# Kernel optimization log

Measured on AMD Instinct MI355X. Metric: run time of the kernel, lower is better.

## Reference

```python
import jax, jax.numpy as jnp
import numpy as np

KS = 7       # neighborhood kernel size (fixed in __init__)
HEADS = 8    # num_heads (fixed in __init__)
LN_EPS = 1e-5


def _nbr_idx(L, k):
    # NATTEN-style clamped window: window start shifts inward at borders (no padding)
    starts = jnp.clip(jnp.arange(L) - k // 2, 0, L - k)
    idx = starts[:, None] + jnp.arange(k)            # [L, k] absolute neighbor coords
    rel = idx - jnp.arange(L)[:, None] + (k - 1)     # [L, k] rel-pos-bias index in [0, 2k-2]
    return idx, rel


def _na2d(x, qkv_w, qkv_b, proj_w, proj_b, rpb):
    # x: [B, H, W, C]  -> neighborhood attention with clamped 7x7 windows
    B, H, W, C = x.shape
    hd = C // HEADS
    qkv = x @ qkv_w.T + qkv_b                        # [B,H,W,3C]
    q, k, v = jnp.split(qkv, 3, axis=-1)
    q = q.reshape(B, H, W, HEADS, hd) * (hd ** -0.5)
    k = k.reshape(B, H, W, HEADS, hd)
    v = v.reshape(B, H, W, HEADS, hd)
    ri, rri = _nbr_idx(H, KS)                        # [H,KS]
    ci, rci = _nbr_idx(W, KS)                        # [W,KS]
    # gather neighborhoods: [B,H,W,KS,KS,heads,hd]
    kn = k[:, ri[:, None, :, None], ci[None, :, None, :]]
    vn = v[:, ri[:, None, :, None], ci[None, :, None, :]]
    scores = jnp.einsum('bijhd,bijpqhd->bhijpq', q, kn)   # [B,heads,H,W,KS,KS]
    bias = rpb[:, rri[:, None, :, None], rci[None, :, None, :]]  # [heads,H,W,KS,KS]
    scores = scores + bias[None]
    attn = jax.nn.softmax(scores.reshape(B, HEADS, H, W, KS * KS), axis=-1)
    vn = vn.reshape(B, H, W, KS * KS, HEADS, hd)
    out = jnp.einsum('bhijp,bijphd->bijhd', attn, vn)      # [B,H,W,heads,hd]
    out = out.reshape(B, H, W, C)
    return out @ proj_w.T + proj_b


def _layernorm(x, g, b):
    mu = jnp.mean(x, axis=-1, keepdims=True)
    var = jnp.mean((x - mu) ** 2, axis=-1, keepdims=True)
    return (x - mu) * jax.lax.rsqrt(var + LN_EPS) * g + b


def setup_inputs() -> dict:
    key = jax.random.key(0)
    ks = jax.random.split(key, 4)
    B, T, H, W, C = 2, 8, 48, 48, 64
    return {
        'q': jax.random.normal(ks[0], (B, T, H, W, C), dtype=jnp.float32),
        'qkv_w': jax.random.normal(ks[1], (3 * C, C), dtype=jnp.float32) * 0.02,
        'qkv_b': jnp.zeros((3 * C,), jnp.float32),
        'proj_w': jax.random.normal(ks[2], (C, C), dtype=jnp.float32) * 0.02,
        'proj_b': jnp.zeros((C,), jnp.float32),
        'rpb': jax.random.normal(ks[3], (HEADS, 2 * KS - 1, 2 * KS - 1), dtype=jnp.float32) * 0.02,
        'ln_g': jnp.ones((C,), jnp.float32),
        'ln_b': jnp.zeros((C,), jnp.float32),
    }


def reference(q, qkv_w, qkv_b, proj_w, proj_b, rpb, ln_g, ln_b):
    B, T, H, W, C = q.shape
    x = q.reshape(B * T, H, W, C)                    # '(b t) h w c'
    x = _na2d(x, qkv_w, qkv_b, proj_w, proj_b, rpb)  # wPT path
    x = x.reshape(B, T, H, W, C)
    return _layernorm(x, ln_g, ln_b)                 # norm_q; wGC=False
```

## Files before the change

kernel.cpp:

```cpp
#include <hip/hip_runtime.h>
#include <hip/hip_bf16.h>

#define IH   48
#define IW   48
#define CH   64
#define KS   7
#define LN_EPS 1e-5f
#define QSCALE 0.35355339059327373f

#define TS   8
#define HS   14
#define HP   196
#define KVS  128
#define AOS  72

typedef __bf16 bf16_t;
typedef bf16_t bf16x8 __attribute__((ext_vector_type(8)));
typedef float  f32x4  __attribute__((ext_vector_type(4)));
typedef float  f32x2  __attribute__((ext_vector_type(2)));

__device__ __forceinline__ float bflo(unsigned u) { union { unsigned i; float f; } v; v.i = u << 16; return v.f; }
__device__ __forceinline__ float bfhi(unsigned u) { union { unsigned i; float f; } v; v.i = u & 0xffff0000u; return v.f; }
__device__ __forceinline__ f32x2 unp2(unsigned u) { f32x2 r; r.x = bflo(u); r.y = bfhi(u); return r; }

__device__ __forceinline__ float4 ldf4u(const float* p) {
    float4 r; __builtin_memcpy(&r, p, 16); return r;
}

__device__ __forceinline__ bf16x8 pack_bf16x8(float4 lo, float4 hi) {
    bf16x8 r;
    r[0] = (bf16_t)lo.x; r[1] = (bf16_t)lo.y; r[2] = (bf16_t)lo.z; r[3] = (bf16_t)lo.w;
    r[4] = (bf16_t)hi.x; r[5] = (bf16_t)hi.y; r[6] = (bf16_t)hi.z; r[7] = (bf16_t)hi.w;
    return r;
}

__global__ __launch_bounds__(256, 2) void fused_na_kernel(
        const float* __restrict__ x,
        const float* __restrict__ w,
        const float* __restrict__ b,
        const float* __restrict__ rpb,
        const float* __restrict__ pw,
        const float* __restrict__ pb,
        const float* __restrict__ g,
        const float* __restrict__ beta,
        float* __restrict__ out) {
    __shared__ __align__(16) __hip_bfloat16 kv[HP * KVS];
    __shared__ __align__(16) __hip_bfloat16 qao[64 * AOS];

    const int blk  = blockIdx.x;
    const int n    = blk & 15;
    const int tile = blk >> 4;
    const int i0   = (tile / 6) * TS;
    const int j0   = (tile % 6) * TS;
    int h0 = i0 - 3; h0 = h0 < 0 ? 0 : (h0 > IH - HS ? IH - HS : h0);
    int w0 = j0 - 3; w0 = w0 < 0 ? 0 : (w0 > IW - HS ? IW - HS : w0);
    const int tid = threadIdx.x;
    const size_t img = (size_t)n * (IH * IW);

    {
        const int wv = tid >> 6;
        const int l  = tid & 63;
        const int m  = l & 15;
        const int kg = l >> 4;

        {
            const int ch_base = m * 4;
            const float4 bias4 = *(const float4*)(b + ch_base);
            bf16x8 wb0[4], wb1[4];
            #pragma unroll
            for (int t = 0; t < 4; ++t) {
                const float* wr_ = w + (size_t)(ch_base + t) * CH + kg * 8;
                wb0[t] = pack_bf16x8(*(const float4*)(wr_),      *(const float4*)(wr_ + 4));
                wb1[t] = pack_bf16x8(*(const float4*)(wr_ + 32), *(const float4*)(wr_ + 36));
            }
            const int px = wv * 16 + m;
            const int hr = i0 + (px >> 3);
            const int wc = j0 + (px & 7);
            const float* xr = x + (img + hr * IW + wc) * CH + kg * 8;
            const bf16x8 a0 = pack_bf16x8(*(const float4*)(xr),      *(const float4*)(xr + 4));
            const bf16x8 a1 = pack_bf16x8(*(const float4*)(xr + 32), *(const float4*)(xr + 36));
            float val[4][4];
            #pragma unroll
            for (int t = 0; t < 4; ++t) {
                f32x4 acc = {0.f, 0.f, 0.f, 0.f};
                acc = __builtin_amdgcn_mfma_f32_16x16x32_bf16(a0, wb0[t], acc, 0, 0, 0);
                acc = __builtin_amdgcn_mfma_f32_16x16x32_bf16(a1, wb1[t], acc, 0, 0, 0);
                const float bias = (t == 0) ? bias4.x : (t == 1) ? bias4.y : (t == 2) ? bias4.z : bias4.w;
                #pragma unroll
                for (int rr = 0; rr < 4; ++rr) val[t][rr] = (acc[rr] + bias) * QSCALE;
            }
            #pragma unroll
            for (int rr = 0; rr < 4; ++rr) {
                const int pix = wv * 16 + kg * 4 + rr;
                union { ushort4 u; __hip_bfloat16 hh[4]; } pk;
                #pragma unroll
                for (int t = 0; t < 4; ++t) pk.hh[t] = __float2bfloat16(val[t][rr]);
                *reinterpret_cast<ushort4*>(qao + pix * 64 + ch_base) = pk.u;
            }
        }

        for (int grp = 1; grp < 3; ++grp) {
            const int ch_base = grp * 64 + m * 4;
            const float4 bias4 = *(const float4*)(b + ch_base);
            bf16x8 wb0[4], wb1[4];
            #pragma unroll
            for (int t = 0; t < 4; ++t) {
                const float* wr_ = w + (size_t)(ch_base + t) * CH + kg * 8;
                wb0[t] = pack_bf16x8(*(const float4*)(wr_),      *(const float4*)(wr_ + 4));
                wb1[t] = pack_bf16x8(*(const float4*)(wr_ + 32), *(const float4*)(wr_ + 36));
            }
            for (int mt = wv; mt < 13; mt += 4) {
                int hp = mt * 16 + m; if (hp > HP - 1) hp = HP - 1;
                const int hr = h0 + hp / HS;
                const int wc = w0 + hp % HS;
                const float* xr = x + (img + hr * IW + wc) * CH + kg * 8;
                const bf16x8 a0 = pack_bf16x8(*(const float4*)(xr),      *(const float4*)(xr + 4));
                const bf16x8 a1 = pack_bf16x8(*(const float4*)(xr + 32), *(const float4*)(xr + 36));
                float val[4][4];
                #pragma unroll
                for (int t = 0; t < 4; ++t) {
                    f32x4 acc = {0.f, 0.f, 0.f, 0.f};
                    acc = __builtin_amdgcn_mfma_f32_16x16x32_bf16(a0, wb0[t], acc, 0, 0, 0);
                    acc = __builtin_amdgcn_mfma_f32_16x16x32_bf16(a1, wb1[t], acc, 0, 0, 0);
                    const float bias = (t == 0) ? bias4.x : (t == 1) ? bias4.y : (t == 2) ? bias4.z : bias4.w;
                    #pragma unroll
                    for (int rr = 0; rr < 4; ++rr) val[t][rr] = acc[rr] + bias;
                }
                #pragma unroll
                for (int rr = 0; rr < 4; ++rr) {
                    const int pix = mt * 16 + kg * 4 + rr;
                    if (pix < HP) {
                        union { ushort4 u; __hip_bfloat16 hh[4]; } pk;
                        #pragma unroll
                        for (int t = 0; t < 4; ++t) pk.hh[t] = __float2bfloat16(val[t][rr]);
                        *reinterpret_cast<ushort4*>(kv + pix * KVS + (grp - 1) * 64 + m * 4) = pk.u;
                    }
                }
            }
        }
    }
    __syncthreads();

    {
        const int h  = tid & 7;
        const int pr = tid >> 3;
        const int pi = pr >> 3;
        const int pj = pr & 7;
        const int i  = i0 + pi * 2;
        const int j  = j0 + pj;
        const int pl0 = pi * 16 + pj;
        const int pl1 = pl0 + 8;

        f32x2 q0[4], q1[4];
        {
            const uint4 u = *reinterpret_cast<const uint4*>(qao + pl0 * 64 + h * 8);
            q0[0] = unp2(u.x); q0[1] = unp2(u.y); q0[2] = unp2(u.z); q0[3] = unp2(u.w);
            const uint4 v = *reinterpret_cast<const uint4*>(qao + pl1 * 64 + h * 8);
            q1[0] = unp2(v.x); q1[1] = unp2(v.y); q1[2] = unp2(v.z); q1[3] = unp2(v.w);
        }
        __syncthreads();

        int si0 = i - 3;     si0 = si0 < 0 ? 0 : (si0 > IH - KS ? IH - KS : si0);
        int si1 = i - 2;     si1 = si1 < 0 ? 0 : (si1 > IH - KS ? IH - KS : si1);
        int sj  = j - 3;     sj  = sj  < 0 ? 0 : (sj  > IW - KS ? IW - KS : sj);
        const int off    = si1 - si0;
        const int rbase0 = si0 - i + 6;
        const float* rpc = rpb + h * (2*KS-1) * (2*KS-1) + (sj - j + (KS - 1));
        const int c0 = sj - w0;

        float lr0 = 0.f, lr1 = 0.f;
        f32x2 a0[4], a1[4];
        #pragma unroll
        for (int d = 0; d < 4; ++d) { a0[d] = (f32x2){0.f,0.f}; a1[d] = (f32x2){0.f,0.f}; }

        for (int p = 0; p < 8; ++p) {
            if (p == 7 && off == 0) break;
            const bool d0 = (p < 7);
            const bool d1 = (p > 0) || (off == 0);
            const __hip_bfloat16* row = kv + ((si0 + p - h0) * HS + c0) * KVS + h * 8;

            uint4 kb[KS], vb[KS];
            #pragma unroll
            for (int qq = 0; qq < KS; ++qq) {
                kb[qq] = *reinterpret_cast<const uint4*>(row + qq * KVS);
                vb[qq] = *reinterpret_cast<const uint4*>(row + qq * KVS + 64);
            }
            float4 r0a = {0,0,0,0}, r0b = {0,0,0,0}, r1a = {0,0,0,0}, r1b = {0,0,0,0};
            if (d0) {
                const float* rr = rpc + (rbase0 + p) * (2*KS-1);
                r0a = ldf4u(rr); r0b = ldf4u(rr + 3);
            }
            if (d1) {
                const float* rr = rpc + (rbase0 - 1 + p) * (2*KS-1);
                r1a = ldf4u(rr); r1b = ldf4u(rr + 3);
            }

            float s0[KS], s1[KS];
            #pragma unroll
            for (int qq = 0; qq < KS; ++qq) {
                const f32x2 k0 = unp2(kb[qq].x), k1 = unp2(kb[qq].y);
                const f32x2 k2 = unp2(kb[qq].z), k3 = unp2(kb[qq].w);
                f32x2 t0 = q0[0]*k0 + q0[1]*k1 + q0[2]*k2 + q0[3]*k3;
                f32x2 t1 = q1[0]*k0 + q1[1]*k1 + q1[2]*k2 + q1[3]*k3;
                s0[qq] = t0.x + t0.y;
                s1[qq] = t1.x + t1.y;
            }
            float e0[KS], e1[KS];
            #pragma unroll
            for (int qq = 0; qq < KS; ++qq) { e0[qq] = 0.f; e1[qq] = 0.f; }
            if (d0) {
                e0[0] = __expf(s0[0] + r0a.x); e0[1] = __expf(s0[1] + r0a.y);
                e0[2] = __expf(s0[2] + r0a.z); e0[3] = __expf(s0[3] + r0a.w);
                e0[4] = __expf(s0[4] + r0b.y); e0[5] = __expf(s0[5] + r0b.z);
                e0[6] = __expf(s0[6] + r0b.w);
            }
            if (d1) {
                e1[0] = __expf(s1[0] + r1a.x); e1[1] = __expf(s1[1] + r1a.y);
                e1[2] = __expf(s1[2] + r1a.z); e1[3] = __expf(s1[3] + r1a.w);
                e1[4] = __expf(s1[4] + r1b.y); e1[5] = __expf(s1[5] + r1b.z);
                e1[6] = __expf(s1[6] + r1b.w);
            }
            #pragma unroll
            for (int qq = 0; qq < KS; ++qq) {
                const f32x2 v0 = unp2(vb[qq].x), v1 = unp2(vb[qq].y);
                const f32x2 v2 = unp2(vb[qq].z), v3 = unp2(vb[qq].w);
                lr0 += e0[qq];
                a0[0] += e0[qq] * v0; a0[1] += e0[qq] * v1;
                a0[2] += e0[qq] * v2; a0[3] += e0[qq] * v3;
                lr1 += e1[qq];
                a1[0] += e1[qq] * v0; a1[1] += e1[qq] * v1;
                a1[2] += e1[qq] * v2; a1[3] += e1[qq] * v3;
            }
        }
        const float inv0 = 1.f / lr0;
        const float inv1 = 1.f / lr1;
        union { uint4 u; __hip_bfloat16 hh[8]; } pk;
        #pragma unroll
        for (int d = 0; d < 4; ++d) {
            pk.hh[2*d]   = __float2bfloat16(a0[d].x * inv0);
            pk.hh[2*d+1] = __float2bfloat16(a0[d].y * inv0);
        }
        *reinterpret_cast<uint4*>(qao + pl0 * AOS + h * 8) = pk.u;
        #pragma unroll
        for (int d = 0; d < 4; ++d) {
            pk.hh[2*d]   = __float2bfloat16(a1[d].x * inv1);
            pk.hh[2*d+1] = __float2bfloat16(a1[d].y * inv1);
        }
        *reinterpret_cast<uint4*>(qao + pl1 * AOS + h * 8) = pk.u;
    }
    __syncthreads();

    {
        const int wv = tid >> 6;
        const int l  = tid & 63;
        const int m  = l & 15;
        const int kg = l >> 4;

        const __hip_bfloat16* ar = qao + (wv * 16 + m) * AOS + kg * 8;
        const bf16x8 a0 = *reinterpret_cast<const bf16x8*>(ar);
        const bf16x8 a1 = *reinterpret_cast<const bf16x8*>(ar + 32);

        const int ch_base = m * 4;
        const float4 bias4 = *(const float4*)(pb + ch_base);

        float val[4][4];
        #pragma unroll
        for (int t = 0; t < 4; ++t) {
            const float* wr_ = pw + (size_t)(ch_base + t) * CH + kg * 8;
            const bf16x8 b0 = pack_bf16x8(*(const float4*)(wr_),      *(const float4*)(wr_ + 4));
            const bf16x8 b1 = pack_bf16x8(*(const float4*)(wr_ + 32), *(const float4*)(wr_ + 36));
            f32x4 acc = {0.f, 0.f, 0.f, 0.f};
            acc = __builtin_amdgcn_mfma_f32_16x16x32_bf16(a0, b0, acc, 0, 0, 0);
            acc = __builtin_amdgcn_mfma_f32_16x16x32_bf16(a1, b1, acc, 0, 0, 0);
            const float bias = (t == 0) ? bias4.x : (t == 1) ? bias4.y : (t == 2) ? bias4.z : bias4.w;
            #pragma unroll
            for (int r = 0; r < 4; ++r) val[t][r] = acc[r] + bias;
        }

        float sm[4];
        #pragma unroll
        for (int r = 0; r < 4; ++r) sm[r] = val[0][r] + val[1][r] + val[2][r] + val[3][r];
        #pragma unroll
        for (int mask = 1; mask <= 8; mask <<= 1) {
            #pragma unroll
            for (int r = 0; r < 4; ++r) sm[r] += __shfl_xor(sm[r], mask, 64);
        }
        float mu[4];
        #pragma unroll
        for (int r = 0; r < 4; ++r) mu[r] = sm[r] * (1.f / 64.f);

        float qs[4];
        #pragma unroll
        for (int r = 0; r < 4; ++r) {
            float a = val[0][r] - mu[r], bq = val[1][r] - mu[r];
            float c = val[2][r] - mu[r], d = val[3][r] - mu[r];
            qs[r] = a * a + bq * bq + c * c + d * d;
        }
        #pragma unroll
        for (int mask = 1; mask <= 8; mask <<= 1) {
            #pragma unroll
            for (int r = 0; r < 4; ++r) qs[r] += __shfl_xor(qs[r], mask, 64);
        }
        float rs[4];
        #pragma unroll
        for (int r = 0; r < 4; ++r) rs[r] = rsqrtf(qs[r] * (1.f / 64.f) + LN_EPS);

        const float4 g4  = *(const float4*)(g + ch_base);
        const float4 be4 = *(const float4*)(beta + ch_base);
        #pragma unroll
        for (int r = 0; r < 4; ++r) {
            const int pl = wv * 16 + kg * 4 + r;
            const int gi = i0 + (pl >> 3), gj = j0 + (pl & 7);
            float4 o;
            o.x = (val[0][r] - mu[r]) * rs[r] * g4.x + be4.x;
            o.y = (val[1][r] - mu[r]) * rs[r] * g4.y + be4.y;
            o.z = (val[2][r] - mu[r]) * rs[r] * g4.z + be4.z;
            o.w = (val[3][r] - mu[r]) * rs[r] * g4.w + be4.w;
            *reinterpret_cast<float4*>(out + (img + gi * IW + gj) * CH + ch_base) = o;
        }
    }
}

extern "C" void kernel_launch(void* const* d_in, const int* in_sizes, int n_in,
                              void* d_out, int out_size, void* d_ws, size_t ws_size,
                              hipStream_t stream) {
    const float* x      = (const float*)d_in[0];
    const float* qkv_w  = (const float*)d_in[1];
    const float* qkv_b  = (const float*)d_in[2];
    const float* proj_w = (const float*)d_in[3];
    const float* proj_b = (const float*)d_in[4];
    const float* rpb    = (const float*)d_in[5];
    const float* ln_g   = (const float*)d_in[6];
    const float* ln_b   = (const float*)d_in[7];
    float* out = (float*)d_out;

    fused_na_kernel<<<576, 256, 0, stream>>>(x, qkv_w, qkv_b, rpb,
                                             proj_w, proj_b, ln_g, ln_b, out);
}
```

Measured before the change: 122.9 us.

## Double block threads to one pixel per thread and use exp2 softmax

Raises the block size from 256 to 512 threads. Each thread now handles one query pixel per head instead of two vertically adjacent pixels that shared K/V row loads, which removes the offset-row predication logic. The K and V projections are split across the two halves of the block, and the Q and output-projection stages run only on the first four waves. The softmax now folds log2(e) into the query scale and bias and uses the native exp2. This trades the earlier reuse of K/V loads across two pixels for more parallelism, at the cost of twice as many LDS reads per output and launch bounds of 512 threads with 4 blocks per CU, which may limit registers.

```diff
diff --git a/kernel.cpp b/kernel.cpp
--- a/kernel.cpp
+++ b/kernel.cpp
@@ -7,6 +7,7 @@
 #define KS   7
 #define LN_EPS 1e-5f
 #define QSCALE 0.35355339059327373f
+#define L2E    1.4426950408889634f
 
 #define TS   8
 #define HS   14
@@ -34,7 +35,7 @@
     return r;
 }
 
-__global__ __launch_bounds__(256, 2) void fused_na_kernel(
+__global__ __launch_bounds__(512, 4) void fused_na_kernel(
         const float* __restrict__ x,
         const float* __restrict__ w,
         const float* __restrict__ b,
@@ -63,7 +64,7 @@
         const int m  = l & 15;
         const int kg = l >> 4;
 
-        {
+        if (wv < 4) {
             const int ch_base = m * 4;
             const float4 bias4 = *(const float4*)(b + ch_base);
             bf16x8 wb0[4], wb1[4];
@@ -87,7 +88,7 @@
                 acc = __builtin_amdgcn_mfma_f32_16x16x32_bf16(a1, wb1[t], acc, 0, 0, 0);
                 const float bias = (t == 0) ? bias4.x : (t == 1) ? bias4.y : (t == 2) ? bias4.z : bias4.w;
                 #pragma unroll
-                for (int rr = 0; rr < 4; ++rr) val[t][rr] = (acc[rr] + bias) * QSCALE;
+                for (int rr = 0; rr < 4; ++rr) val[t][rr] = (acc[rr] + bias) * (QSCALE * L2E);
             }
             #pragma unroll
             for (int rr = 0; rr < 4; ++rr) {
@@ -99,7 +100,8 @@
             }
         }
 
-        for (int grp = 1; grp < 3; ++grp) {
+        {
+            const int grp = 1 + (wv >> 2);
             const int ch_base = grp * 64 + m * 4;
             const float4 bias4 = *(const float4*)(b + ch_base);
             bf16x8 wb0[4], wb1[4];
@@ -109,7 +111,7 @@
                 wb0[t] = pack_bf16x8(*(const float4*)(wr_),      *(const float4*)(wr_ + 4));
                 wb1[t] = pack_bf16x8(*(const float4*)(wr_ + 32), *(const float4*)(wr_ + 36));
             }
-            for (int mt = wv; mt < 13; mt += 4) {
+            for (int mt = wv & 3; mt < 13; mt += 4) {
                 int hp = mt * 16 + m; if (hp > HP - 1) hp = HP - 1;
                 const int hr = h0 + hp / HS;
                 const int wc = w0 + hp % HS;
@@ -143,114 +145,78 @@
 
     {
         const int h  = tid & 7;
-        const int pr = tid >> 3;
-        const int pi = pr >> 3;
-        const int pj = pr & 7;
-        const int i  = i0 + pi * 2;
-        const int j  = j0 + pj;
-        const int pl0 = pi * 16 + pj;
-        const int pl1 = pl0 + 8;
-
-        f32x2 q0[4], q1[4];
+        const int px = tid >> 3;
+        const int i  = i0 + (px >> 3);
+        const int j  = j0 + (px & 7);
+
+        f32x2 q0[4];
         {
-            const uint4 u = *reinterpret_cast<const uint4*>(qao + pl0 * 64 + h * 8);
+            const uint4 u = *reinterpret_cast<const uint4*>(qao + px * 64 + h * 8);
             q0[0] = unp2(u.x); q0[1] = unp2(u.y); q0[2] = unp2(u.z); q0[3] = unp2(u.w);
-            const uint4 v = *reinterpret_cast<const uint4*>(qao + pl1 * 64 + h * 8);
-            q1[0] = unp2(v.x); q1[1] = unp2(v.y); q1[2] = unp2(v.z); q1[3] = unp2(v.w);
         }
         __syncthreads();
 
-        int si0 = i - 3;     si0 = si0 < 0 ? 0 : (si0 > IH - KS ? IH - KS : si0);
-        int si1 = i - 2;     si1 = si1 < 0 ? 0 : (si1 > IH - KS ? IH - KS : si1);
-        int sj  = j - 3;     sj  = sj  < 0 ? 0 : (sj  > IW - KS ? IW - KS : sj);
-        const int off    = si1 - si0;
-        const int rbase0 = si0 - i + 6;
-        const float* rpc = rpb + h * (2*KS-1) * (2*KS-1) + (sj - j + (KS - 1));
-        const int c0 = sj - w0;
-
-        float lr0 = 0.f, lr1 = 0.f;
-        f32x2 a0[4], a1[4];
-        #pragma unroll
-        for (int d = 0; d < 4; ++d) { a0[d] = (f32x2){0.f,0.f}; a1[d] = (f32x2){0.f,0.f}; }
-
-        for (int p = 0; p < 8; ++p) {
-            if (p == 7 && off == 0) break;
-            const bool d0 = (p < 7);
-            const bool d1 = (p > 0) || (off == 0);
-            const __hip_bfloat16* row = kv + ((si0 + p - h0) * HS + c0) * KVS + h * 8;
-
+        int si = i - 3;  si = si < 0 ? 0 : (si > IH - KS ? IH - KS : si);
+        int sj = j - 3;  sj = sj < 0 ? 0 : (sj > IW - KS ? IW - KS : sj);
+        const float* rpc = rpb + h * (2*KS-1) * (2*KS-1)
+                               + (si - i + (KS-1)) * (2*KS-1) + (sj - j + (KS-1));
+        const __hip_bfloat16* kbase = kv + ((si - h0) * HS + (sj - w0)) * KVS + h * 8;
+
+        float lr = 0.f;
+        f32x2 a[4];
+        #pragma unroll
+        for (int d = 0; d < 4; ++d) a[d] = (f32x2){0.f, 0.f};
+
+        for (int p = 0; p < KS; ++p) {
+            const __hip_bfloat16* row = kbase + p * (HS * KVS);
             uint4 kb[KS], vb[KS];
             #pragma unroll
             for (int qq = 0; qq < KS; ++qq) {
                 kb[qq] = *reinterpret_cast<const uint4*>(row + qq * KVS);
                 vb[qq] = *reinterpret_cast<const uint4*>(row + qq * KVS + 64);
             }
-            float4 r0a = {0,0,0,0}, r0b = {0,0,0,0}, r1a = {0,0,0,0}, r1b = {0,0,0,0};
-            if (d0) {
-                const float* rr = rpc + (rbase0 + p) * (2*KS-1);
-                r0a = ldf4u(rr); r0b = ldf4u(rr + 3);
-            }
-            if (d1) {
-                const float* rr = rpc + (rbase0 - 1 + p) * (2*KS-1);
-                r1a = ldf4u(rr); r1b = ldf4u(rr + 3);
-            }
-
-            float s0[KS], s1[KS];
+            const float* rr = rpc + p * (2*KS-1);
+            const float4 ba = ldf4u(rr);
+            const float4 bb = ldf4u(rr + 3);
+
+            float s[KS];
             #pragma unroll
             for (int qq = 0; qq < KS; ++qq) {
                 const f32x2 k0 = unp2(kb[qq].x), k1 = unp2(kb[qq].y);
                 const f32x2 k2 = unp2(kb[qq].z), k3 = unp2(kb[qq].w);
-                f32x2 t0 = q0[0]*k0 + q0[1]*k1 + q0[2]*k2 + q0[3]*k3;
-                f32x2 t1 = q1[0]*k0 + q1[1]*k1 + q1[2]*k2 + q1[3]*k3;
-                s0[qq] = t0.x + t0.y;
-                s1[qq] = t1.x + t1.y;
-            }
-            float e0[KS], e1[KS];
-            #pragma unroll
-            for (int qq = 0; qq < KS; ++qq) { e0[qq] = 0.f; e1[qq] = 0.f; }
-            if (d0) {
-                e0[0] = __expf(s0[0] + r0a.x); e0[1] = __expf(s0[1] + r0a.y);
-                e0[2] = __expf(s0[2] + r0a.z); e0[3] = __expf(s0[3] + r0a.w);
-                e0[4] = __expf(s0[4] + r0b.y); e0[5] = __expf(s0[5] + r0b.z);
-                e0[6] = __expf(s0[6] + r0b.w);
-            }
-            if (d1) {
-                e1[0] = __expf(s1[0] + r1a.x); e1[1] = __expf(s1[1] + r1a.y);
-                e1[2] = __expf(s1[2] + r1a.z); e1[3] = __expf(s1[3] + r1a.w);
-                e1[4] = __expf(s1[4] + r1b.y); e1[5] = __expf(s1[5] + r1b.z);
-                e1[6] = __expf(s1[6] + r1b.w);
-            }
+                f32x2 t = q0[0]*k0 + q0[1]*k1 + q0[2]*k2 + q0[3]*k3;
+                s[qq] = t.x + t.y;
+            }
+            float e[KS];
+            e[0] = __builtin_amdgcn_exp2f(fmaf(ba.x, L2E, s[0]));
+            e[1] = __builtin_amdgcn_exp2f(fmaf(ba.y, L2E, s[1]));
+            e[2] = __builtin_amdgcn_exp2f(fmaf(ba.z, L2E, s[2]));
+            e[3] = __builtin_amdgcn_exp2f(fmaf(ba.w, L2E, s[3]));
+            e[4] = __builtin_amdgcn_exp2f(fmaf(bb.y, L2E, s[4]));
+            e[5] = __builtin_amdgcn_exp2f(fmaf(bb.z, L2E, s[5]));
+            e[6] = __builtin_amdgcn_exp2f(fmaf(bb.w, L2E, s[6]));
+
             #pragma unroll
             for (int qq = 0; qq < KS; ++qq) {
                 const f32x2 v0 = unp2(vb[qq].x), v1 = unp2(vb[qq].y);
                 const f32x2 v2 = unp2(vb[qq].z), v3 = unp2(vb[qq].w);
-                lr0 += e0[qq];
-                a0[0] += e0[qq] * v0; a0[1] += e0[qq] * v1;
-                a0[2] += e0[qq] * v2; a0[3] += e0[qq] * v3;
-                lr1 += e1[qq];
-                a1[0] += e1[qq] * v0; a1[1] += e1[qq] * v1;
-                a1[2] += e1[qq] * v2; a1[3] += e1[qq] * v3;
-            }
-        }
-        const float inv0 = 1.f / lr0;
-        const float inv1 = 1.f / lr1;
+                lr += e[qq];
+                a[0] += e[qq] * v0; a[1] += e[qq] * v1;
+                a[2] += e[qq] * v2; a[3] += e[qq] * v3;
+            }
+        }
+        const float inv = 1.f / lr;
         union { uint4 u; __hip_bfloat16 hh[8]; } pk;
         #pragma unroll
         for (int d = 0; d < 4; ++d) {
-            pk.hh[2*d]   = __float2bfloat16(a0[d].x * inv0);
-            pk.hh[2*d+1] = __float2bfloat16(a0[d].y * inv0);
-        }
-        *reinterpret_cast<uint4*>(qao + pl0 * AOS + h * 8) = pk.u;
-        #pragma unroll
-        for (int d = 0; d < 4; ++d) {
-            pk.hh[2*d]   = __float2bfloat16(a1[d].x * inv1);
-            pk.hh[2*d+1] = __float2bfloat16(a1[d].y * inv1);
-        }
-        *reinterpret_cast<uint4*>(qao + pl1 * AOS + h * 8) = pk.u;
+            pk.hh[2*d]   = __float2bfloat16(a[d].x * inv);
+            pk.hh[2*d+1] = __float2bfloat16(a[d].y * inv);
+        }
+        *reinterpret_cast<uint4*>(qao + px * AOS + h * 8) = pk.u;
     }
     __syncthreads();
 
-    {
+    if ((tid >> 6) < 4) {
         const int wv = tid >> 6;
         const int l  = tid & 63;
         const int m  = l & 15;
@@ -292,9 +258,9 @@
         float qs[4];
         #pragma unroll
         for (int r = 0; r < 4; ++r) {
-            float a = val[0][r] - mu[r], bq = val[1][r] - mu[r];
-            float c = val[2][r] - mu[r], d = val[3][r] - mu[r];
-            qs[r] = a * a + bq * bq + c * c + d * d;
+            float aa = val[0][r] - mu[r], bq = val[1][r] - mu[r];
+            float c  = val[2][r] - mu[r], d  = val[3][r] - mu[r];
+            qs[r] = aa * aa + bq * bq + c * c + d * d;
         }
         #pragma unroll
         for (int mask = 1; mask <= 8; mask <<= 1) {
@@ -334,6 +300,6 @@
     const float* ln_b   = (const float*)d_in[7];
     float* out = (float*)d_out;
 
-    fused_na_kernel<<<576, 256, 0, stream>>>(x, qkv_w, qkv_b, rpb,
+    fused_na_kernel<<<576, 512, 0, stream>>>(x, qkv_w, qkv_b, rpb,
                                              proj_w, proj_b, ln_g, ln_b, out);
 }
```

New measurement: 118.9 us. 1.03x faster.
